# Performance work log

Measured on AMD Instinct MI355X. Metric: run time of the kernel, lower is better.

Reference implementation:

```python
import jax, jax.numpy as jnp
import numpy as np

STOCH, DETER, HID, OBS, ACT = 32, 512, 512, 18, 4
MIN_STD, EPS, UPD_BIAS = 0.1, 1e-3, -1.0


def _ln(x, g, b):
    m = x.mean(-1, keepdims=True)
    v = ((x - m) ** 2).mean(-1, keepdims=True)
    return (x - m) * jax.lax.rsqrt(v + EPS) * g + b


def setup_inputs() -> dict:
    key = jax.random.key(0)
    ks = jax.random.split(key, 10)
    B, T = 256, 256
    def w(k, i, o):
        return jax.random.normal(k, (i, o), jnp.float32) / np.float32(np.sqrt(i))
    return {
        "obs": jax.random.normal(ks[0], (B, T, OBS), jnp.float32),
        "action": jax.random.normal(ks[1], (B, T, ACT), jnp.float32),
        "is_first": jax.random.randint(ks[2], (B, T), 0, 2, jnp.int32),
        "w_prior_in": w(ks[3], STOCH + ACT, HID),
        "g_prior_in": jnp.ones(HID, jnp.float32),
        "bb_prior_in": jnp.zeros(HID, jnp.float32),
        "w_gru": w(ks[4], HID + DETER, 3 * DETER),
        "g_gru": jnp.ones(3 * DETER, jnp.float32),
        "bb_gru": jnp.zeros(3 * DETER, jnp.float32),
        "w_prior_out": w(ks[5], DETER, HID),
        "g_prior_out": jnp.ones(HID, jnp.float32),
        "bb_prior_out": jnp.zeros(HID, jnp.float32),
        "w_prior_stats": w(ks[6], HID, 2 * STOCH),
        "b_prior_stats": jnp.zeros(2 * STOCH, jnp.float32),
        "w_post": w(ks[7], DETER + OBS, HID),
        "g_post": jnp.ones(HID, jnp.float32),
        "bb_post": jnp.zeros(HID, jnp.float32),
        "w_post_stats": w(ks[8], HID, 2 * STOCH),
        "b_post_stats": jnp.zeros(2 * STOCH, jnp.float32),
        "initial_deter": 0.1 * jax.random.normal(ks[9], (1, DETER), jnp.float32),
    }


def reference(obs, action, is_first,
              w_prior_in, g_prior_in, bb_prior_in,
              w_gru, g_gru, bb_gru,
              w_prior_out, g_prior_out, bb_prior_out,
              w_prior_stats, b_prior_stats,
              w_post, g_post, bb_post,
              w_post_stats, b_post_stats,
              initial_deter):
    """RSSM.observe with sample=False. Returns (B, T, 2*(DETER+3*STOCH)):
    concat of post[deter,stoch,mean,std] and prior[deter,stoch,mean,std];
    stoch == mean since dist.mean is used."""
    B = obs.shape[0]
    # learned initial state (identical for every batch row / reset)
    deter0 = jnp.tanh(initial_deter)                                  # (1, DETER)
    h0 = jax.nn.silu(_ln(deter0 @ w_prior_out, g_prior_out, bb_prior_out))
    s0 = h0 @ w_prior_stats + b_prior_stats
    init_mean, _ = jnp.split(s0, 2, axis=-1)                          # (1, STOCH)

    def step(carry, xs):
        deter, stoch = carry
        o_t, a_t, f_t = xs
        mask = (f_t > 0)[:, None]
        deter = jnp.where(mask, deter0, deter)
        stoch = jnp.where(mask, init_mean, stoch)
        a_t = jnp.where(mask, 0.0, a_t)
        # prior_in
        h = jax.nn.silu(_ln(jnp.concatenate([stoch, a_t], -1) @ w_prior_in,
                            g_prior_in, bb_prior_in))
        # GRU cell (depth=1)
        gates = _ln(jnp.concatenate([h, deter], -1) @ w_gru, g_gru, bb_gru)
        r, c, u = jnp.split(gates, 3, axis=-1)
        r = jax.nn.sigmoid(r)
        u = jax.nn.sigmoid(u + UPD_BIAS)
        cand = jax.nn.silu(r * c)
        deter = u * cand + (1.0 - u) * deter
        # prior stats
        h2 = jax.nn.silu(_ln(deter @ w_prior_out, g_prior_out, bb_prior_out))
        ps = h2 @ w_prior_stats + b_prior_stats
        pm, psd = jnp.split(ps, 2, axis=-1)
        psd = jax.nn.softplus(psd) + MIN_STD
        # posterior
        h3 = jax.nn.silu(_ln(jnp.concatenate([deter, o_t], -1) @ w_post,
                             g_post, bb_post))
        qs = h3 @ w_post_stats + b_post_stats
        qm, qsd = jnp.split(qs, 2, axis=-1)
        qsd = jax.nn.softplus(qsd) + MIN_STD
        out = jnp.concatenate([deter, qm, qm, qsd, deter, pm, pm, psd], -1)
        return (deter, qm), out

    carry0 = (jnp.broadcast_to(deter0, (B, DETER)),
              jnp.broadcast_to(init_mean, (B, STOCH)))
    xs = (obs.swapaxes(0, 1), action.swapaxes(0, 1), is_first.swapaxes(0, 1))
    _, ys = jax.lax.scan(step, carry0, xs)   # (T, B, 2*(DETER+3*STOCH))
    return ys.swapaxes(0, 1)
```

## Files before the change

### kernel.cpp

```cpp
#include <hip/hip_runtime.h>
#include <hip/hip_cooperative_groups.h>

namespace cg = cooperative_groups;

#define TT 256
#define GRID 256
#define BDIM 256

typedef unsigned short u16;
typedef unsigned int u32;
typedef __attribute__((ext_vector_type(8))) short bf16x8;
typedef __attribute__((ext_vector_type(4))) float f32x4;

#define GLL(g, l) __builtin_amdgcn_global_load_lds( \
    (const __attribute__((address_space(1))) void*)(g), \
    (__attribute__((address_space(3))) void*)(l), 16, 0, 0)

struct P {
  const float* obs; const float* action; const int* is_first;
  const float* w_prior_in; const float* g_prior_in; const float* bb_prior_in;
  const float* w_gru; const float* g_gru; const float* bb_gru;
  const float* w_prior_out; const float* g_prior_out; const float* bb_prior_out;
  const float* w_prior_stats; const float* b_prior_stats;
  const float* w_post; const float* g_post; const float* bb_post;
  const float* w_post_stats; const float* b_post_stats;
  const float* initial_deter;
  float* out;
  u16 *WgT3;
  u16 *W2T3;
  u16 *WsT3;
  float *deter0, *init_mean;
  int *segb, *segt0, *nact;
  float *deter;
  float *stoch;
  u16 *xg;
  float *gates;
  u16 *dox;
  float *hraw;
  u16 *h2;
  int CH;
};

__device__ __forceinline__ float b2f(u16 u) {
  union { float f; u32 i; } v; v.i = ((u32)u) << 16; return v.f;
}
__device__ __forceinline__ u16 f2b(float f) {
  union { float f; u32 i; } v; v.f = f;
  u32 r = v.i + 0x7FFF + ((v.i >> 16) & 1);
  return (u16)(r >> 16);
}
__device__ __forceinline__ float sigm(float x) { return 1.f / (1.f + __expf(-x)); }
__device__ __forceinline__ float splus(float x) { return x > 15.f ? x : log1pf(__expf(x)); }

__device__ __forceinline__ void h_from_x(const P& p, int i, float xv, int lane) {
  float a0[8];
  #pragma unroll
  for (int c = 0; c < 8; ++c) a0[c] = 0.f;
  #pragma unroll 4
  for (int j = 0; j < 36; ++j) {
    float s = __shfl(xv, j, 64);
    const float* wr = p.w_prior_in + j * 512 + lane;
    #pragma unroll
    for (int c = 0; c < 8; ++c) a0[c] = fmaf(s, wr[c << 6], a0[c]);
  }
  float sm = 0.f, sq = 0.f;
  #pragma unroll
  for (int c = 0; c < 8; ++c) { sm += a0[c]; sq += a0[c] * a0[c]; }
  #pragma unroll
  for (int o = 32; o; o >>= 1) { sm += __shfl_xor(sm, o); sq += __shfl_xor(sq, o); }
  float m = sm * (1.f / 512.f);
  float rs = rsqrtf(sq * (1.f / 512.f) - m * m + 1e-3f);
  size_t rowb = (size_t)i * 3072;
  #pragma unroll
  for (int c = 0; c < 8; ++c) {
    int col = lane + (c << 6);
    float v = (a0[c] - m) * rs * p.g_prior_in[col] + p.bb_prior_in[col];
    v = v * sigm(v);
    u16 hi = f2b(v); u16 lo = f2b(v - b2f(hi));
    p.xg[rowb + col] = hi;
    p.xg[rowb + 1024 + col] = lo;
    p.xg[rowb + 2048 + col] = hi;
  }
}

__global__ void k_weights(P p) {
  const int E1 = 1536 * 1024, E2 = 1024 * 544, E3 = 128 * 1024;
  const int total = E1 + E2 + E3;
  for (int idx = blockIdx.x * blockDim.x + threadIdx.x; idx < total;
       idx += gridDim.x * blockDim.x) {
    float w; u16* dst; int kk, kappa;
    if (idx < E1) {
      int n = idx >> 10; kk = idx & 1023; kappa = 1024;
      w = p.w_gru[kk * 1536 + n];
      dst = p.WgT3 + (size_t)n * 3072;
    } else if (idx < E1 + E2) {
      int t = idx - E1; int n = t / 544; kk = t - n * 544; kappa = 544;
      if (n < 512) w = (kk < 512) ? p.w_prior_out[kk * 512 + n] : 0.f;
      else         w = (kk < 530) ? p.w_post[kk * 512 + (n - 512)] : 0.f;
      dst = p.W2T3 + (size_t)n * 1632;
    } else {
      int t = idx - E1 - E2; int n = t >> 10; kk = t & 1023; kappa = 1024;
      if (n < 64) w = (kk < 512) ? p.w_prior_stats[kk * 64 + n] : 0.f;
      else        w = (kk >= 512) ? p.w_post_stats[(kk - 512) * 64 + (n - 64)] : 0.f;
      dst = p.WsT3 + (size_t)n * 3072;
    }
    u16 hi = f2b(w); u16 lo = f2b(w - b2f(hi));
    dst[kk] = hi; dst[kappa + kk] = hi; dst[2 * kappa + kk] = lo;
  }
}

__global__ void k_init_state(P p) {
  __shared__ float d0s[512], tmp[512], red[256];
  int tid = threadIdx.x;
  for (int n = tid; n < 512; n += 256) { d0s[n] = tanhf(p.initial_deter[n]); p.deter0[n] = d0s[n]; }
  __syncthreads();
  for (int n = tid; n < 512; n += 256) {
    float s = 0.f;
    for (int d = 0; d < 512; ++d) s = fmaf(d0s[d], p.w_prior_out[d * 512 + n], s);
    tmp[n] = s;
  }
  __syncthreads();
  float ls = 0.f, lq = 0.f;
  for (int n = tid; n < 512; n += 256) { ls += tmp[n]; lq += tmp[n] * tmp[n]; }
  red[tid] = ls; __syncthreads();
  for (int s = 128; s; s >>= 1) { if (tid < s) red[tid] += red[tid + s]; __syncthreads(); }
  float m = red[0] * (1.f / 512.f); __syncthreads();
  red[tid] = lq; __syncthreads();
  for (int s = 128; s; s >>= 1) { if (tid < s) red[tid] += red[tid + s]; __syncthreads(); }
  float rs = rsqrtf(red[0] * (1.f / 512.f) - m * m + 1e-3f); __syncthreads();
  for (int n = tid; n < 512; n += 256) {
    float h = (tmp[n] - m) * rs * p.g_prior_out[n] + p.bb_prior_out[n];
    tmp[n] = h * sigm(h);
  }
  __syncthreads();
  if (tid < 32) {
    float s = 0.f;
    for (int d = 0; d < 512; ++d) s = fmaf(tmp[d], p.w_prior_stats[d * 64 + tid], s);
    p.init_mean[tid] = s + p.b_prior_stats[tid];
  }
}

__global__ void k_segments(P p) {
  __shared__ int hist[257], off[258], cur[257];
  int tid = threadIdx.x;
  for (int i = tid; i < 257; i += 256) hist[i] = 0;
  __syncthreads();
  int b = tid;
  { int t = 0;
    while (t < TT) {
      int t0 = t; t++;
      while (t < TT && p.is_first[b * TT + t] == 0) t++;
      atomicAdd(&hist[t - t0], 1);
    } }
  __syncthreads();
  if (tid == 0) {
    int run = 0;
    for (int len = 256; len >= 0; --len) { off[len] = run; run += hist[len]; }
  }
  __syncthreads();
  for (int i = tid; i < 257; i += 256) { cur[i] = off[i]; p.nact[i] = off[i]; }
  __syncthreads();
  { int t = 0;
    while (t < TT) {
      int t0 = t; t++;
      while (t < TT && p.is_first[b * TT + t] == 0) t++;
      int idx = atomicAdd(&cur[t - t0], 1);
      p.segb[idx] = b; p.segt0[idx] = t0;
    } }
}

__device__ void gemm_tiles(const u16* A, int lda, const u16* B, int ldb,
                           float* C, int ldc, int M, int ntn, int K3,
                           u16* lds, int bid, int nb, int tid) {
  const int wave = tid >> 6, lane = tid & 63, quad = lane >> 4, l15 = lane & 15;
  const int wr = (wave & 1) << 6, wc = (wave >> 1) << 6;
  const int ntm = (M + 127) >> 7;
  const int njobs = ntm * ntn;
  const int row0 = tid >> 2, ko0 = (tid & 3) << 3;
  u16* const la0 = lds + (wave << 9);
  u16* const la1 = lds + 2048 + (wave << 9);
  u16* const lb0 = lds + 8192 + (wave << 9);
  u16* const lb1 = lds + 8192 + 2048 + (wave << 9);
  for (int j = bid; j < njobs; j += nb) {
    int tm = j / ntn, tn = j - tm * ntn;
    int r0 = tm << 7, c0 = tn << 7;
    const u16* ga0 = A + (size_t)(r0 + row0) * lda + ko0;
    const u16* ga1 = A + (size_t)(r0 + row0 + 64) * lda + ko0;
    const u16* gb0 = B + (size_t)(c0 + row0) * ldb + ko0;
    const u16* gb1 = B + (size_t)(c0 + row0 + 64) * ldb + ko0;
    f32x4 acc[4][4];
    #pragma unroll
    for (int a = 0; a < 4; ++a)
      #pragma unroll
      for (int bq = 0; bq < 4; ++bq) acc[a][bq] = f32x4{0.f, 0.f, 0.f, 0.f};
    __syncthreads();
    GLL(ga0, la0); GLL(ga1, la1); GLL(gb0, lb0); GLL(gb1, lb1);
    int buf = 0;
    for (int k0 = 0; k0 < K3; k0 += 32) {
      __syncthreads();
      if (k0 + 32 < K3) {
        int bo = (buf ^ 1) << 12;
        int o = k0 + 32;
        GLL(ga0 + o, la0 + bo); GLL(ga1 + o, la1 + bo);
        GLL(gb0 + o, lb0 + bo); GLL(gb1 + o, lb1 + bo);
      }
      const u16* Ab = lds + (buf << 12);
      const u16* Bb = lds + 8192 + (buf << 12);
      bf16x8 af[4], bf[4];
      #pragma unroll
      for (int s2 = 0; s2 < 4; ++s2) {
        af[s2] = *(const bf16x8*)&Ab[((wr + (s2 << 4) + l15) << 5) + (quad << 3)];
        bf[s2] = *(const bf16x8*)&Bb[((wc + (s2 << 4) + l15) << 5) + (quad << 3)];
      }
      #pragma unroll
      for (int mi = 0; mi < 4; ++mi)
        #pragma unroll
        for (int ni = 0; ni < 4; ++ni)
          acc[mi][ni] = __builtin_amdgcn_mfma_f32_16x16x32_bf16(af[mi], bf[ni], acc[mi][ni], 0, 0, 0);
      buf ^= 1;
    }
    #pragma unroll
    for (int mi = 0; mi < 4; ++mi)
      #pragma unroll
      for (int ni = 0; ni < 4; ++ni)
        #pragma unroll
        for (int r = 0; r < 4; ++r)
          C[(size_t)(r0 + wr + (mi << 4) + (quad << 2) + r) * ldc
            + c0 + wc + (ni << 4) + l15] = acc[mi][ni][r];
  }
}

__global__ void __launch_bounds__(BDIM, 2) k_main(P p) {
  cg::grid_group grid = cg::this_grid();
  __shared__ u16 lds[16384];
  const int tid = threadIdx.x;
  const int bid = blockIdx.x, nb = gridDim.x;
  const int wave = tid >> 6, lane = tid & 63, quad = lane >> 4, l15 = lane & 15;
  const int gw = (bid << 2) + wave, nwv = nb << 2;
  const int CH = p.CH;
  const int S_total = p.nact[0];

  for (int base = 0; base < S_total; base += CH) {
    for (int k = 0;; ++k) {
      int Sk = p.nact[k] - base; Sk = Sk > CH ? CH : Sk;
      if (Sk <= 0) break;

      for (int i = gw; i < Sk; i += nwv) {
        int gi = base + i;
        int b = p.segb[gi], t0 = p.segt0[gi];
        float xv = 0.f;
        if (k == 0) {
          size_t rowb = (size_t)i * 3072;
          #pragma unroll
          for (int c = 0; c < 8; ++c) {
            int d = lane + (c << 6);
            float v = p.deter0[d];
            p.deter[(size_t)i * 512 + d] = v;
            u16 hi = f2b(v); u16 lo = f2b(v - b2f(hi));
            p.xg[rowb + 512 + d] = hi;
            p.xg[rowb + 1536 + d] = lo;
            p.xg[rowb + 2560 + d] = hi;
          }
          int ff = p.is_first[b * TT + t0];
          if (lane < 32) xv = p.init_mean[lane];
          else if (lane < 36) xv = (ff > 0) ? 0.f : p.action[((size_t)b * TT + t0) * 4 + (lane - 32)];
        } else {
          if (lane < 32) xv = p.stoch[(size_t)i * 32 + lane];
          else if (lane < 36) xv = p.action[((size_t)b * TT + t0 + k) * 4 + (lane - 32)];
        }
        h_from_x(p, i, xv, lane);
      }
      grid.sync();

      gemm_tiles(p.xg, 3072, p.WgT3, 3072, p.gates, 1536, Sk, 12, 3072,
                 lds, bid, nb, tid);
      grid.sync();

      for (int i = gw; i < Sk; i += nwv) {
        const float* grow = p.gates + (size_t)i * 1536;
        float g[24];
        float sm = 0.f, sq = 0.f;
        #pragma unroll
        for (int c = 0; c < 24; ++c) {
          g[c] = grow[lane + (c << 6)];
          sm += g[c]; sq += g[c] * g[c];
        }
        #pragma unroll
        for (int o = 32; o; o >>= 1) { sm += __shfl_xor(sm, o); sq += __shfl_xor(sq, o); }
        float m = sm * (1.f / 1536.f);
        float rs = rsqrtf(sq * (1.f / 1536.f) - m * m + 1e-3f);
        int gi = base + i;
        int b = p.segb[gi], t = p.segt0[gi] + k;
        float* orow = p.out + ((size_t)b * TT + t) * 1216;
        size_t rowx = (size_t)i * 3072, rowd = (size_t)i * 1632;
        #pragma unroll
        for (int c = 0; c < 8; ++c) {
          int d = lane + (c << 6);
          float gr = (g[c]      - m) * rs * p.g_gru[d]        + p.bb_gru[d];
          float gc = (g[c + 8]  - m) * rs * p.g_gru[512 + d]  + p.bb_gru[512 + d];
          float gu = (g[c + 16] - m) * rs * p.g_gru[1024 + d] + p.bb_gru[1024 + d];
          float r_ = sigm(gr);
          float u_ = sigm(gu - 1.0f);
          float rc = r_ * gc;
          float cand = rc * sigm(rc);
          float dp = p.deter[(size_t)i * 512 + d];
          float dn = u_ * cand + (1.f - u_) * dp;
          p.deter[(size_t)i * 512 + d] = dn;
          orow[d] = dn; orow[608 + d] = dn;
          u16 hi = f2b(dn); u16 lo = f2b(dn - b2f(hi));
          p.xg[rowx + 512 + d] = hi;
          p.xg[rowx + 1536 + d] = lo;
          p.xg[rowx + 2560 + d] = hi;
          p.dox[rowd + d] = hi;
          p.dox[rowd + 544 + d] = lo;
          p.dox[rowd + 1088 + d] = hi;
        }
        if (lane < 32) {
          float ov = (lane < 18) ? p.obs[((size_t)b * TT + t) * 18 + lane] : 0.f;
          u16 hi = f2b(ov); u16 lo = f2b(ov - b2f(hi));
          p.dox[rowd + 512 + lane] = hi;
          p.dox[rowd + 1056 + lane] = lo;
          p.dox[rowd + 1600 + lane] = hi;
        }
      }
      grid.sync();

      gemm_tiles(p.dox, 1632, p.W2T3, 1632, p.hraw, 1024, Sk, 8, 1632,
                 lds, bid, nb, tid);
      grid.sync();

      for (int i = gw; i < Sk; i += nwv) {
        size_t rowh = (size_t)i * 3072;
        #pragma unroll
        for (int hh = 0; hh < 2; ++hh) {
          const float* hb = p.hraw + (size_t)i * 1024 + (hh << 9);
          const float* gv = hh ? p.g_post : p.g_prior_out;
          const float* bv = hh ? p.bb_post : p.bb_prior_out;
          float v[8];
          float sm = 0.f, sq = 0.f;
          #pragma unroll
          for (int c = 0; c < 8; ++c) {
            v[c] = hb[lane + (c << 6)];
            sm += v[c]; sq += v[c] * v[c];
          }
          #pragma unroll
          for (int o = 32; o; o >>= 1) { sm += __shfl_xor(sm, o); sq += __shfl_xor(sq, o); }
          float m = sm * (1.f / 512.f);
          float rs = rsqrtf(sq * (1.f / 512.f) - m * m + 1e-3f);
          #pragma unroll
          for (int c = 0; c < 8; ++c) {
            int d = lane + (c << 6);
            float x = (v[c] - m) * rs * gv[d] + bv[d];
            x = x * sigm(x);
            int col = (hh << 9) + d;
            u16 hi = f2b(x); u16 lo = f2b(x - b2f(hi));
            p.h2[rowh + col] = hi;
            p.h2[rowh + 1024 + col] = lo;
            p.h2[rowh + 2048 + col] = hi;
          }
        }
      }
      grid.sync();

      {
        const int sr = (wave & 1) << 4, sc = (wave >> 1) << 6;
        const int frow = tid >> 2, fko = (tid & 3) << 3;
        int njobs = (Sk + 31) >> 5;
        const u16* gbF0 = p.WsT3 + (size_t)frow * 3072 + fko;
        const u16* gbF1 = p.WsT3 + (size_t)(frow + 64) * 3072 + fko;
        u16* const lFA = lds + (wave << 9);
        u16* const lFB0 = lds + 2048 + (wave << 9);
        u16* const lFB1 = lds + 2048 + 2048 + (wave << 9);
        for (int j = bid; j < njobs; j += nb) {
          int r0 = j << 5;
          const u16* gaF = p.h2 + (size_t)(r0 + frow) * 3072 + fko;
          f32x4 acc[4];
          #pragma unroll
          for (int z = 0; z < 4; ++z) acc[z] = f32x4{0.f, 0.f, 0.f, 0.f};
          __syncthreads();
          if (tid < 128) GLL(gaF, lFA);
          GLL(gbF0, lFB0); GLL(gbF1, lFB1);
          int buf = 0;
          for (int k0 = 0; k0 < 3072; k0 += 32) {
            __syncthreads();
            if (k0 + 32 < 3072) {
              int nbuf = buf ^ 1;
              int o = k0 + 32;
              if (tid < 128) GLL(gaF + o, lFA + (nbuf << 10));
              GLL(gbF0 + o, lFB0 + (nbuf << 12));
              GLL(gbF1 + o, lFB1 + (nbuf << 12));
            }
            const u16* FA = lds + (buf << 10);
            const u16* FB = lds + 2048 + (buf << 12);
            bf16x8 af = *(const bf16x8*)&FA[((sr + l15) << 5) + (quad << 3)];
            #pragma unroll
            for (int ns = 0; ns < 4; ++ns) {
              bf16x8 bf = *(const bf16x8*)&FB[((sc + (ns << 4) + l15) << 5) + (quad << 3)];
              acc[ns] = __builtin_amdgcn_mfma_f32_16x16x32_bf16(af, bf, acc[ns], 0, 0, 0);
            }
            buf ^= 1;
          }
          #pragma unroll
          for (int ns = 0; ns < 4; ++ns)
            #pragma unroll
            for (int r = 0; r < 4; ++r) {
              int i = r0 + sr + (quad << 2) + r;
              int col = sc + (ns << 4) + l15;
              if (i < Sk) {
                float v = acc[ns][r];
                int gi = base + i;
                int b = p.segb[gi], t = p.segt0[gi] + k;
                float* orow = p.out + ((size_t)b * TT + t) * 1216;
                if (col < 32) {
                  v += p.b_prior_stats[col];
                  orow[1120 + col] = v; orow[1152 + col] = v;
                } else if (col < 64) {
                  v = splus(v + p.b_prior_stats[col]) + 0.1f;
                  orow[1184 + col - 32] = v;
                } else if (col < 96) {
                  v += p.b_post_stats[col - 64];
                  orow[512 + col - 64] = v; orow[544 + col - 64] = v;
                  p.stoch[(size_t)i * 32 + (col - 64)] = v;
                } else {
                  v = splus(v + p.b_post_stats[col - 64]) + 0.1f;
                  orow[576 + col - 96] = v;
                }
              }
            }
        }
      }
      grid.sync();
    }
  }
}

extern "C" void kernel_launch(void* const* d_in, const int* in_sizes, int n_in,
                              void* d_out, int out_size, void* d_ws, size_t ws_size,
                              hipStream_t stream) {
  P p;
  p.obs = (const float*)d_in[0];
  p.action = (const float*)d_in[1];
  p.is_first = (const int*)d_in[2];
  p.w_prior_in = (const float*)d_in[3];
  p.g_prior_in = (const float*)d_in[4];
  p.bb_prior_in = (const float*)d_in[5];
  p.w_gru = (const float*)d_in[6];
  p.g_gru = (const float*)d_in[7];
  p.bb_gru = (const float*)d_in[8];
  p.w_prior_out = (const float*)d_in[9];
  p.g_prior_out = (const float*)d_in[10];
  p.bb_prior_out = (const float*)d_in[11];
  p.w_prior_stats = (const float*)d_in[12];
  p.b_prior_stats = (const float*)d_in[13];
  p.w_post = (const float*)d_in[14];
  p.g_post = (const float*)d_in[15];
  p.bb_post = (const float*)d_in[16];
  p.w_post_stats = (const float*)d_in[17];
  p.b_post_stats = (const float*)d_in[18];
  p.initial_deter = (const float*)d_in[19];
  p.out = (float*)d_out;

  char* w = (char*)d_ws;
  auto alloc = [&](size_t bytes) -> char* {
    char* r = w; w += (bytes + 255) & ~(size_t)255; return r;
  };
  p.WgT3 = (u16*)alloc((size_t)1536 * 3072 * 2);
  p.W2T3 = (u16*)alloc((size_t)1024 * 1632 * 2);
  p.WsT3 = (u16*)alloc((size_t)128 * 3072 * 2);
  p.deter0    = (float*)alloc(512 * 4);
  p.init_mean = (float*)alloc(32 * 4);
  p.segb  = (int*)alloc((size_t)65536 * 4);
  p.segt0 = (int*)alloc((size_t)65536 * 4);
  p.nact  = (int*)alloc(257 * 4);
  size_t used = (size_t)(w - (char*)d_ws);
  size_t avail = ws_size > used ? ws_size - used : 0;
  long long ch = (long long)(avail / 28672);
  if (ch > 8192) ch = 8192;
  ch &= ~127LL;
  if (ch < 128) ch = 128;
  p.CH = (int)ch;
  p.deter = (float*)alloc((size_t)p.CH * 512 * 4);
  p.stoch = (float*)alloc((size_t)p.CH * 32 * 4);
  p.xg    = (u16*)alloc((size_t)p.CH * 3072 * 2);
  p.gates = (float*)alloc((size_t)p.CH * 1536 * 4);
  p.dox   = (u16*)alloc((size_t)p.CH * 1632 * 2);
  p.hraw  = (float*)alloc((size_t)p.CH * 1024 * 4);
  p.h2    = (u16*)alloc((size_t)p.CH * 3072 * 2);

  k_weights<<<dim3(256), dim3(256), 0, stream>>>(p);
  k_init_state<<<dim3(1), dim3(256), 0, stream>>>(p);
  k_segments<<<dim3(1), dim3(256), 0, stream>>>(p);
  void* args[] = { &p };
  hipLaunchCooperativeKernel(reinterpret_cast<void*>(&k_main), dim3(GRID), dim3(BDIM),
                             args, 0, stream);
}
```

Before: 10.61 ms.

## Replace grid-synced chunked GEMMs with per-block 32-row tiles from an atomic queue

The cooperative kernel, which ran every timestep with grid-wide syncs and 128x128 GEMM tiles over all active rows, is replaced. Each block now pulls 32-row tiles of sorted segments from an atomic work queue and runs the whole recurrence for them locally, using only block barriers. Weights and activations are pre-laid-out in 32-column K-chunks with an XOR swizzle, and each GEMM uses a triple-buffered global-to-LDS pipeline with explicit vmcnt waits. This removes grid-sync latency but makes every block stream the full weight set for each tile and timestep, which adds weight traffic and leaves load balance to the queue.

```diff
diff --git a/kernel.cpp b/kernel.cpp
--- a/kernel.cpp
+++ b/kernel.cpp
@@ -1,11 +1,8 @@
 #include <hip/hip_runtime.h>
-#include <hip/hip_cooperative_groups.h>
-
-namespace cg = cooperative_groups;
 
 #define TT 256
-#define GRID 256
 #define BDIM 256
+#define MT 32
 
 typedef unsigned short u16;
 typedef unsigned int u32;
@@ -30,15 +27,14 @@
   u16 *W2T3;
   u16 *WsT3;
   float *deter0, *init_mean;
-  int *segb, *segt0, *nact;
+  int *segb, *segt0, *nact, *qhead;
+  u16 *arow;
+  u16 *h2;
+  float *gates;
+  float *hraw;
   float *deter;
   float *stoch;
-  u16 *xg;
-  float *gates;
-  u16 *dox;
-  float *hraw;
-  u16 *h2;
-  int CH;
+  int NB;
 };
 
 __device__ __forceinline__ float b2f(u16 u) {
@@ -52,7 +48,11 @@
 __device__ __forceinline__ float sigm(float x) { return 1.f / (1.f + __expf(-x)); }
 __device__ __forceinline__ float splus(float x) { return x > 15.f ? x : log1pf(__expf(x)); }
 
-__device__ __forceinline__ void h_from_x(const P& p, int i, float xv, int lane) {
+__device__ __forceinline__ void awr(u16* base, int row, int kk, u16 v) {
+  base[((kk >> 5) << 10) + (((row << 5) + (kk & 31)) ^ ((row & 7) << 3))] = v;
+}
+
+__device__ __forceinline__ void h_from_x(const P& p, u16* slotA, int i, float xv, int lane) {
   float a0[8];
   #pragma unroll
   for (int c = 0; c < 8; ++c) a0[c] = 0.f;
@@ -70,42 +70,59 @@
   for (int o = 32; o; o >>= 1) { sm += __shfl_xor(sm, o); sq += __shfl_xor(sq, o); }
   float m = sm * (1.f / 512.f);
   float rs = rsqrtf(sq * (1.f / 512.f) - m * m + 1e-3f);
-  size_t rowb = (size_t)i * 3072;
   #pragma unroll
   for (int c = 0; c < 8; ++c) {
     int col = lane + (c << 6);
     float v = (a0[c] - m) * rs * p.g_prior_in[col] + p.bb_prior_in[col];
     v = v * sigm(v);
     u16 hi = f2b(v); u16 lo = f2b(v - b2f(hi));
-    p.xg[rowb + col] = hi;
-    p.xg[rowb + 1024 + col] = lo;
-    p.xg[rowb + 2048 + col] = hi;
+    awr(slotA, i, 1536 + col, hi);
+    awr(slotA, i, 2048 + col, lo);
+    awr(slotA, i, 2560 + col, hi);
   }
 }
 
 __global__ void k_weights(P p) {
-  const int E1 = 1536 * 1024, E2 = 1024 * 544, E3 = 128 * 1024;
+  const int E1 = 1536 * 3072, E2 = 1024 * 1632, E3 = 128 * 3072;
   const int total = E1 + E2 + E3;
   for (int idx = blockIdx.x * blockDim.x + threadIdx.x; idx < total;
        idx += gridDim.x * blockDim.x) {
-    float w; u16* dst; int kk, kappa;
+    float w; u16* base; size_t dstIdx; int lo_sel;
     if (idx < E1) {
-      int n = idx >> 10; kk = idx & 1023; kappa = 1024;
-      w = p.w_gru[kk * 1536 + n];
-      dst = p.WgT3 + (size_t)n * 3072;
+      int n = idx / 3072, kk = idx - n * 3072;
+      int sub = (kk < 1536) ? kk : kk - 1536;
+      int c = sub & 511, pl = sub >> 9;
+      w = (kk < 1536) ? p.w_gru[(512 + c) * 1536 + n]
+                      : p.w_gru[c * 1536 + n];
+      lo_sel = (pl == 2);
+      base = p.WgT3;
+      dstIdx = (size_t)(kk >> 5) * 49152 + (((n << 5) + (kk & 31)) ^ ((n & 7) << 3));
     } else if (idx < E1 + E2) {
-      int t = idx - E1; int n = t / 544; kk = t - n * 544; kappa = 544;
-      if (n < 512) w = (kk < 512) ? p.w_prior_out[kk * 512 + n] : 0.f;
-      else         w = (kk < 530) ? p.w_post[kk * 512 + (n - 512)] : 0.f;
-      dst = p.W2T3 + (size_t)n * 1632;
+      int t = idx - E1;
+      int n = t / 1632, kk = t - n * 1632;
+      if (kk < 1536) {
+        int c = kk & 511, pl = kk >> 9;
+        w = (n < 512) ? p.w_prior_out[c * 512 + n] : p.w_post[c * 512 + (n - 512)];
+        lo_sel = (pl == 2);
+      } else {
+        int j = kk - 1536; int c = j & 31, pl = j >> 5;
+        w = (n >= 512 && c < 18) ? p.w_post[(512 + c) * 512 + (n - 512)] : 0.f;
+        lo_sel = (pl == 2);
+      }
+      base = p.W2T3;
+      dstIdx = (size_t)(kk >> 5) * 32768 + (((n << 5) + (kk & 31)) ^ ((n & 7) << 3));
     } else {
-      int t = idx - E1 - E2; int n = t >> 10; kk = t & 1023; kappa = 1024;
-      if (n < 64) w = (kk < 512) ? p.w_prior_stats[kk * 64 + n] : 0.f;
-      else        w = (kk >= 512) ? p.w_post_stats[(kk - 512) * 64 + (n - 64)] : 0.f;
-      dst = p.WsT3 + (size_t)n * 3072;
+      int t = idx - E1 - E2;
+      int n = t / 3072, kk = t - n * 3072;
+      int c = kk & 1023, pl = kk >> 10;
+      if (n < 64) w = (c < 512) ? p.w_prior_stats[c * 64 + n] : 0.f;
+      else        w = (c >= 512) ? p.w_post_stats[(c - 512) * 64 + (n - 64)] : 0.f;
+      lo_sel = (pl == 2);
+      base = p.WsT3;
+      dstIdx = (size_t)(kk >> 5) * 4096 + (((n << 5) + (kk & 31)) ^ ((n & 7) << 3));
     }
     u16 hi = f2b(w); u16 lo = f2b(w - b2f(hi));
-    dst[kk] = hi; dst[kappa + kk] = hi; dst[2 * kappa + kk] = lo;
+    base[dstIdx] = lo_sel ? lo : hi;
   }
 }
 
@@ -143,6 +160,7 @@
 __global__ void k_segments(P p) {
   __shared__ int hist[257], off[258], cur[257];
   int tid = threadIdx.x;
+  if (tid == 0) *p.qhead = 0;
   for (int i = tid; i < 257; i += 256) hist[i] = 0;
   __syncthreads();
   int b = tid;
@@ -169,171 +187,206 @@
     } }
 }
 
-__device__ void gemm_tiles(const u16* A, int lda, const u16* B, int ldb,
-                           float* C, int ldc, int M, int ntn, int K3,
-                           u16* lds, int bid, int nb, int tid) {
-  const int wave = tid >> 6, lane = tid & 63, quad = lane >> 4, l15 = lane & 15;
-  const int wr = (wave & 1) << 6, wc = (wave >> 1) << 6;
-  const int ntm = (M + 127) >> 7;
-  const int njobs = ntm * ntn;
-  const int row0 = tid >> 2, ko0 = (tid & 3) << 3;
-  u16* const la0 = lds + (wave << 9);
-  u16* const la1 = lds + 2048 + (wave << 9);
-  u16* const lb0 = lds + 8192 + (wave << 9);
-  u16* const lb1 = lds + 8192 + 2048 + (wave << 9);
-  for (int j = bid; j < njobs; j += nb) {
-    int tm = j / ntn, tn = j - tm * ntn;
-    int r0 = tm << 7, c0 = tn << 7;
-    const u16* ga0 = A + (size_t)(r0 + row0) * lda + ko0;
-    const u16* ga1 = A + (size_t)(r0 + row0 + 64) * lda + ko0;
-    const u16* gb0 = B + (size_t)(c0 + row0) * ldb + ko0;
-    const u16* gb1 = B + (size_t)(c0 + row0 + 64) * ldb + ko0;
-    f32x4 acc[4][4];
+template<int NI, int NSTEPS, int JAT, int JD>
+__device__ __forceinline__ void gemm_pass(
+    const u16* __restrict__ aBase, const u16* __restrict__ wBase,
+    int wStride, int n0, u16* ldsA, u16* ldsW,
+    int wave, int lane, int quad, int l15, f32x4 (&acc)[2][NI]) {
+
+  auto stage = [&](int st, int buf) {
+    int ach = (JAT < NSTEPS && st >= JAT) ? st + JD : st;
+    const u16* aSrc = aBase + ((size_t)ach << 10) + (wave << 9) + (lane << 3);
+    const u16* wSrc = wBase + (size_t)st * wStride + n0 * 32 + (lane << 3);
+    if (wave < 2) GLL(aSrc, ldsA + buf * 1024 + (wave << 9));
     #pragma unroll
-    for (int a = 0; a < 4; ++a)
-      #pragma unroll
-      for (int bq = 0; bq < 4; ++bq) acc[a][bq] = f32x4{0.f, 0.f, 0.f, 0.f};
-    __syncthreads();
-    GLL(ga0, la0); GLL(ga1, la1); GLL(gb0, lb0); GLL(gb1, lb1);
-    int buf = 0;
-    for (int k0 = 0; k0 < K3; k0 += 32) {
-      __syncthreads();
-      if (k0 + 32 < K3) {
-        int bo = (buf ^ 1) << 12;
-        int o = k0 + 32;
-        GLL(ga0 + o, la0 + bo); GLL(ga1 + o, la1 + bo);
-        GLL(gb0 + o, lb0 + bo); GLL(gb1 + o, lb1 + bo);
-      }
-      const u16* Ab = lds + (buf << 12);
-      const u16* Bb = lds + 8192 + (buf << 12);
-      bf16x8 af[4], bf[4];
-      #pragma unroll
-      for (int s2 = 0; s2 < 4; ++s2) {
-        af[s2] = *(const bf16x8*)&Ab[((wr + (s2 << 4) + l15) << 5) + (quad << 3)];
-        bf[s2] = *(const bf16x8*)&Bb[((wc + (s2 << 4) + l15) << 5) + (quad << 3)];
-      }
-      #pragma unroll
-      for (int mi = 0; mi < 4; ++mi)
-        #pragma unroll
-        for (int ni = 0; ni < 4; ++ni)
-          acc[mi][ni] = __builtin_amdgcn_mfma_f32_16x16x32_bf16(af[mi], bf[ni], acc[mi][ni], 0, 0, 0);
-      buf ^= 1;
+    for (int gg = 0; gg < NI; ++gg) {
+      int g = wave * NI + gg;
+      GLL(wSrc + (g << 9), ldsW + buf * 8192 + (g << 9));
+    }
+  };
+  auto compute = [&](int buf) {
+    const u16* A = ldsA + buf * 1024;
+    const u16* W = ldsW + buf * 8192;
+    int xr = (l15 & 7) << 3;
+    bf16x8 af[2];
+    #pragma unroll
+    for (int mi = 0; mi < 2; ++mi) {
+      int r = mi * 16 + l15;
+      af[mi] = *(const bf16x8*)&A[((r << 5) + (quad << 3)) ^ xr];
     }
     #pragma unroll
-    for (int mi = 0; mi < 4; ++mi)
+    for (int ni = 0; ni < NI; ++ni) {
+      int rr = wave * (NI * 16) + ni * 16 + l15;
+      bf16x8 bv = *(const bf16x8*)&W[((rr << 5) + (quad << 3)) ^ xr];
       #pragma unroll
-      for (int ni = 0; ni < 4; ++ni)
-        #pragma unroll
-        for (int r = 0; r < 4; ++r)
-          C[(size_t)(r0 + wr + (mi << 4) + (quad << 2) + r) * ldc
-            + c0 + wc + (ni << 4) + l15] = acc[mi][ni][r];
-  }
-}
-
-__global__ void __launch_bounds__(BDIM, 2) k_main(P p) {
-  cg::grid_group grid = cg::this_grid();
-  __shared__ u16 lds[16384];
+      for (int mi = 0; mi < 2; ++mi)
+        acc[mi][ni] = __builtin_amdgcn_mfma_f32_16x16x32_bf16(af[mi], bv, acc[mi][ni], 0, 0, 0);
+    }
+  };
+
+  stage(0, 0); stage(1, 1);
+  int b3 = 0;
+  for (int st = 0; st < NSTEPS - 1; ++st) {
+    if (wave < 2) asm volatile("s_waitcnt vmcnt(%0)" :: "i"(NI + 1) : "memory");
+    else          asm volatile("s_waitcnt vmcnt(%0)" :: "i"(NI) : "memory");
+    __builtin_amdgcn_s_barrier();
+    __builtin_amdgcn_sched_barrier(0);
+    if (st + 2 < NSTEPS) {
+      int bs = b3 + 2; if (bs >= 3) bs -= 3;
+      stage(st + 2, bs);
+    }
+    compute(b3);
+    ++b3; if (b3 == 3) b3 = 0;
+  }
+  asm volatile("s_waitcnt vmcnt(0)" ::: "memory");
+  __builtin_amdgcn_s_barrier();
+  __builtin_amdgcn_sched_barrier(0);
+  compute(b3);
+}
+
+__global__ void __launch_bounds__(BDIM) k_main(P p) {
+  __shared__ u16 lds[27648];
+  __shared__ int sg;
   const int tid = threadIdx.x;
-  const int bid = blockIdx.x, nb = gridDim.x;
   const int wave = tid >> 6, lane = tid & 63, quad = lane >> 4, l15 = lane & 15;
-  const int gw = (bid << 2) + wave, nwv = nb << 2;
-  const int CH = p.CH;
+  u16* ldsA = lds;
+  u16* ldsW = lds + 3072;
+  const int blk = blockIdx.x;
+  u16* slotA = p.arow + (size_t)blk * 102400;
+  u16* slotH = p.h2 + (size_t)blk * 98304;
+  float* slotG = p.gates + (size_t)blk * 49152;
+  float* slotR = p.hraw + (size_t)blk * 32768;
+  float* slotD = p.deter + (size_t)blk * 16384;
+  float* slotS = p.stoch + (size_t)blk * 1024;
   const int S_total = p.nact[0];
-
-  for (int base = 0; base < S_total; base += CH) {
+  const int ntiles = (S_total + MT - 1) >> 5;
+
+  for (;;) {
+    __syncthreads();
+    if (tid == 0) sg = atomicAdd(p.qhead, 1);
+    __syncthreads();
+    int g = sg;
+    if (g >= ntiles) return;
+    int row0 = g * MT;
+    int nr0 = S_total - row0; if (nr0 > MT) nr0 = MT;
+
     for (int k = 0;; ++k) {
-      int Sk = p.nact[k] - base; Sk = Sk > CH ? CH : Sk;
-      if (Sk <= 0) break;
-
-      for (int i = gw; i < Sk; i += nwv) {
-        int gi = base + i;
+      int Mk = p.nact[k] - row0; if (Mk > nr0) Mk = nr0;
+      if (Mk <= 0) break;
+
+      for (int i = wave; i < Mk; i += 4) {
+        int gi = row0 + i;
         int b = p.segb[gi], t0 = p.segt0[gi];
         float xv = 0.f;
         if (k == 0) {
-          size_t rowb = (size_t)i * 3072;
           #pragma unroll
           for (int c = 0; c < 8; ++c) {
             int d = lane + (c << 6);
             float v = p.deter0[d];
-            p.deter[(size_t)i * 512 + d] = v;
+            slotD[i * 512 + d] = v;
             u16 hi = f2b(v); u16 lo = f2b(v - b2f(hi));
-            p.xg[rowb + 512 + d] = hi;
-            p.xg[rowb + 1536 + d] = lo;
-            p.xg[rowb + 2560 + d] = hi;
+            awr(slotA, i, d, hi);
+            awr(slotA, i, 512 + d, lo);
+            awr(slotA, i, 1024 + d, hi);
           }
           int ff = p.is_first[b * TT + t0];
           if (lane < 32) xv = p.init_mean[lane];
           else if (lane < 36) xv = (ff > 0) ? 0.f : p.action[((size_t)b * TT + t0) * 4 + (lane - 32)];
         } else {
-          if (lane < 32) xv = p.stoch[(size_t)i * 32 + lane];
+          if (lane < 32) xv = slotS[i * 32 + lane];
           else if (lane < 36) xv = p.action[((size_t)b * TT + t0 + k) * 4 + (lane - 32)];
         }
-        h_from_x(p, i, xv, lane);
-      }
-      grid.sync();
-
-      gemm_tiles(p.xg, 3072, p.WgT3, 3072, p.gates, 1536, Sk, 12, 3072,
-                 lds, bid, nb, tid);
-      grid.sync();
-
-      for (int i = gw; i < Sk; i += nwv) {
-        const float* grow = p.gates + (size_t)i * 1536;
-        float g[24];
+        h_from_x(p, slotA, i, xv, lane);
+      }
+      __syncthreads();
+
+      for (int np = 0; np < 6; ++np) {
+        f32x4 acc[2][4];
+        #pragma unroll
+        for (int a = 0; a < 2; ++a)
+          #pragma unroll
+          for (int bq = 0; bq < 4; ++bq) acc[a][bq] = f32x4{0.f, 0.f, 0.f, 0.f};
+        gemm_pass<4, 96, 1000, 0>(slotA, p.WgT3, 49152, np * 256,
+                                  ldsA, ldsW, wave, lane, quad, l15, acc);
+        #pragma unroll
+        for (int mi = 0; mi < 2; ++mi)
+          #pragma unroll
+          for (int ni = 0; ni < 4; ++ni)
+            #pragma unroll
+            for (int r = 0; r < 4; ++r)
+              slotG[(mi * 16 + quad * 4 + r) * 1536 + np * 256 + wave * 64 + ni * 16 + l15]
+                  = acc[mi][ni][r];
+      }
+      __syncthreads();
+
+      for (int i = wave; i < Mk; i += 4) {
+        const float* grow = slotG + i * 1536;
+        float g24[24];
         float sm = 0.f, sq = 0.f;
         #pragma unroll
         for (int c = 0; c < 24; ++c) {
-          g[c] = grow[lane + (c << 6)];
-          sm += g[c]; sq += g[c] * g[c];
+          g24[c] = grow[lane + (c << 6)];
+          sm += g24[c]; sq += g24[c] * g24[c];
         }
         #pragma unroll
         for (int o = 32; o; o >>= 1) { sm += __shfl_xor(sm, o); sq += __shfl_xor(sq, o); }
         float m = sm * (1.f / 1536.f);
         float rs = rsqrtf(sq * (1.f / 1536.f) - m * m + 1e-3f);
-        int gi = base + i;
+        int gi = row0 + i;
         int b = p.segb[gi], t = p.segt0[gi] + k;
         float* orow = p.out + ((size_t)b * TT + t) * 1216;
-        size_t rowx = (size_t)i * 3072, rowd = (size_t)i * 1632;
         #pragma unroll
         for (int c = 0; c < 8; ++c) {
           int d = lane + (c << 6);
-          float gr = (g[c]      - m) * rs * p.g_gru[d]        + p.bb_gru[d];
-          float gc = (g[c + 8]  - m) * rs * p.g_gru[512 + d]  + p.bb_gru[512 + d];
-          float gu = (g[c + 16] - m) * rs * p.g_gru[1024 + d] + p.bb_gru[1024 + d];
+          float gr = (g24[c] - m) * rs * p.g_gru[d] + p.bb_gru[d];
+          float gc = (g24[c + 8] - m) * rs * p.g_gru[512 + d] + p.bb_gru[512 + d];
+          float gu = (g24[c + 16] - m) * rs * p.g_gru[1024 + d] + p.bb_gru[1024 + d];
           float r_ = sigm(gr);
           float u_ = sigm(gu - 1.0f);
           float rc = r_ * gc;
           float cand = rc * sigm(rc);
-          float dp = p.deter[(size_t)i * 512 + d];
+          float dp = slotD[i * 512 + d];
           float dn = u_ * cand + (1.f - u_) * dp;
-          p.deter[(size_t)i * 512 + d] = dn;
+          slotD[i * 512 + d] = dn;
           orow[d] = dn; orow[608 + d] = dn;
           u16 hi = f2b(dn); u16 lo = f2b(dn - b2f(hi));
-          p.xg[rowx + 512 + d] = hi;
-          p.xg[rowx + 1536 + d] = lo;
-          p.xg[rowx + 2560 + d] = hi;
-          p.dox[rowd + d] = hi;
-          p.dox[rowd + 544 + d] = lo;
-          p.dox[rowd + 1088 + d] = hi;
+          awr(slotA, i, d, hi);
+          awr(slotA, i, 512 + d, lo);
+          awr(slotA, i, 1024 + d, hi);
         }
         if (lane < 32) {
           float ov = (lane < 18) ? p.obs[((size_t)b * TT + t) * 18 + lane] : 0.f;
           u16 hi = f2b(ov); u16 lo = f2b(ov - b2f(hi));
-          p.dox[rowd + 512 + lane] = hi;
-          p.dox[rowd + 1056 + lane] = lo;
-          p.dox[rowd + 1600 + lane] = hi;
+          awr(slotA, i, 3072 + lane, hi);
+          awr(slotA, i, 3104 + lane, lo);
+          awr(slotA, i, 3136 + lane, hi);
         }
       }
-      grid.sync();
-
-      gemm_tiles(p.dox, 1632, p.W2T3, 1632, p.hraw, 1024, Sk, 8, 1632,
-                 lds, bid, nb, tid);
-      grid.sync();
-
-      for (int i = gw; i < Sk; i += nwv) {
-        size_t rowh = (size_t)i * 3072;
+      __syncthreads();
+
+      for (int np = 0; np < 4; ++np) {
+        f32x4 acc[2][4];
+        #pragma unroll
+        for (int a = 0; a < 2; ++a)
+          #pragma unroll
+          for (int bq = 0; bq < 4; ++bq) acc[a][bq] = f32x4{0.f, 0.f, 0.f, 0.f};
+        gemm_pass<4, 51, 48, 48>(slotA, p.W2T3, 32768, np * 256,
+                                 ldsA, ldsW, wave, lane, quad, l15, acc);
+        #pragma unroll
+        for (int mi = 0; mi < 2; ++mi)
+          #pragma unroll
+          for (int ni = 0; ni < 4; ++ni)
+            #pragma unroll
+            for (int r = 0; r < 4; ++r)
+              slotR[(mi * 16 + quad * 4 + r) * 1024 + np * 256 + wave * 64 + ni * 16 + l15]
+                  = acc[mi][ni][r];
+      }
+      __syncthreads();
+
+      for (int i = wave; i < Mk; i += 4) {
         #pragma unroll
         for (int hh = 0; hh < 2; ++hh) {
-          const float* hb = p.hraw + (size_t)i * 1024 + (hh << 9);
+          const float* hb = slotR + i * 1024 + (hh << 9);
           const float* gv = hh ? p.g_post : p.g_prior_out;
           const float* bv = hh ? p.bb_post : p.bb_prior_out;
           float v[8];
@@ -354,61 +407,33 @@
             x = x * sigm(x);
             int col = (hh << 9) + d;
             u16 hi = f2b(x); u16 lo = f2b(x - b2f(hi));
-            p.h2[rowh + col] = hi;
-            p.h2[rowh + 1024 + col] = lo;
-            p.h2[rowh + 2048 + col] = hi;
+            awr(slotH, i, col, hi);
+            awr(slotH, i, 1024 + col, lo);
+            awr(slotH, i, 2048 + col, hi);
           }
         }
       }
-      grid.sync();
+      __syncthreads();
 
       {
-        const int sr = (wave & 1) << 4, sc = (wave >> 1) << 6;
-        const int frow = tid >> 2, fko = (tid & 3) << 3;
-        int njobs = (Sk + 31) >> 5;
-        const u16* gbF0 = p.WsT3 + (size_t)frow * 3072 + fko;
-        const u16* gbF1 = p.WsT3 + (size_t)(frow + 64) * 3072 + fko;
-        u16* const lFA = lds + (wave << 9);
-        u16* const lFB0 = lds + 2048 + (wave << 9);
-        u16* const lFB1 = lds + 2048 + 2048 + (wave << 9);
-        for (int j = bid; j < njobs; j += nb) {
-          int r0 = j << 5;
-          const u16* gaF = p.h2 + (size_t)(r0 + frow) * 3072 + fko;
-          f32x4 acc[4];
-          #pragma unroll
-          for (int z = 0; z < 4; ++z) acc[z] = f32x4{0.f, 0.f, 0.f, 0.f};
-          __syncthreads();
-          if (tid < 128) GLL(gaF, lFA);
-          GLL(gbF0, lFB0); GLL(gbF1, lFB1);
-          int buf = 0;
-          for (int k0 = 0; k0 < 3072; k0 += 32) {
-            __syncthreads();
-            if (k0 + 32 < 3072) {
-              int nbuf = buf ^ 1;
-              int o = k0 + 32;
-              if (tid < 128) GLL(gaF + o, lFA + (nbuf << 10));
-              GLL(gbF0 + o, lFB0 + (nbuf << 12));
-              GLL(gbF1 + o, lFB1 + (nbuf << 12));
-            }
-            const u16* FA = lds + (buf << 10);
-            const u16* FB = lds + 2048 + (buf << 12);
-            bf16x8 af = *(const bf16x8*)&FA[((sr + l15) << 5) + (quad << 3)];
-            #pragma unroll
-            for (int ns = 0; ns < 4; ++ns) {
-              bf16x8 bf = *(const bf16x8*)&FB[((sc + (ns << 4) + l15) << 5) + (quad << 3)];
-              acc[ns] = __builtin_amdgcn_mfma_f32_16x16x32_bf16(af, bf, acc[ns], 0, 0, 0);
-            }
-            buf ^= 1;
-          }
-          #pragma unroll
-          for (int ns = 0; ns < 4; ++ns)
+        f32x4 acc[2][2];
+        #pragma unroll
+        for (int a = 0; a < 2; ++a)
+          #pragma unroll
+          for (int bq = 0; bq < 2; ++bq) acc[a][bq] = f32x4{0.f, 0.f, 0.f, 0.f};
+        gemm_pass<2, 96, 1000, 0>(slotH, p.WsT3, 4096, 0,
+                                  ldsA, ldsW, wave, lane, quad, l15, acc);
+        #pragma unroll
+        for (int mi = 0; mi < 2; ++mi)
+          #pragma unroll
+          for (int ni = 0; ni < 2; ++ni)
             #pragma unroll
             for (int r = 0; r < 4; ++r) {
-              int i = r0 + sr + (quad << 2) + r;
-              int col = sc + (ns << 4) + l15;
-              if (i < Sk) {
-                float v = acc[ns][r];
-                int gi = base + i;
+              int i = mi * 16 + quad * 4 + r;
+              int col = wave * 32 + ni * 16 + l15;
+              if (i < Mk) {
+                float v = acc[mi][ni][r];
+                int gi = row0 + i;
                 int b = p.segb[gi], t = p.segt0[gi] + k;
                 float* orow = p.out + ((size_t)b * TT + t) * 1216;
                 if (col < 32) {
@@ -420,16 +445,15 @@
                 } else if (col < 96) {
                   v += p.b_post_stats[col - 64];
                   orow[512 + col - 64] = v; orow[544 + col - 64] = v;
-                  p.stoch[(size_t)i * 32 + (col - 64)] = v;
+                  slotS[i * 32 + (col - 64)] = v;
                 } else {
                   v = splus(v + p.b_post_stats[col - 64]) + 0.1f;
                   orow[576 + col - 96] = v;
                 }
               }
             }
-        }
-      }
-      grid.sync();
+      }
+      __syncthreads();
     }
   }
 }
@@ -467,30 +491,28 @@
   p.WgT3 = (u16*)alloc((size_t)1536 * 3072 * 2);
   p.W2T3 = (u16*)alloc((size_t)1024 * 1632 * 2);
   p.WsT3 = (u16*)alloc((size_t)128 * 3072 * 2);
-  p.deter0    = (float*)alloc(512 * 4);
+  p.deter0 = (float*)alloc(512 * 4);
   p.init_mean = (float*)alloc(32 * 4);
-  p.segb  = (int*)alloc((size_t)65536 * 4);
+  p.segb = (int*)alloc((size_t)65536 * 4);
   p.segt0 = (int*)alloc((size_t)65536 * 4);
-  p.nact  = (int*)alloc(257 * 4);
+  p.nact = (int*)alloc(257 * 4);
+  p.qhead = (int*)alloc(256);
   size_t used = (size_t)(w - (char*)d_ws);
   size_t avail = ws_size > used ? ws_size - used : 0;
-  long long ch = (long long)(avail / 28672);
-  if (ch > 8192) ch = 8192;
-  ch &= ~127LL;
-  if (ch < 128) ch = 128;
-  p.CH = (int)ch;
-  p.deter = (float*)alloc((size_t)p.CH * 512 * 4);
-  p.stoch = (float*)alloc((size_t)p.CH * 32 * 4);
-  p.xg    = (u16*)alloc((size_t)p.CH * 3072 * 2);
-  p.gates = (float*)alloc((size_t)p.CH * 1536 * 4);
-  p.dox   = (u16*)alloc((size_t)p.CH * 1632 * 2);
-  p.hraw  = (float*)alloc((size_t)p.CH * 1024 * 4);
-  p.h2    = (u16*)alloc((size_t)p.CH * 3072 * 2);
+  size_t slot = 800768;
+  long long nb = (long long)(avail / slot);
+  if (nb > 256) nb = 256;
+  if (nb < 1) nb = 1;
+  p.NB = (int)nb;
+  p.arow = (u16*)alloc((size_t)p.NB * 204800);
+  p.h2 = (u16*)alloc((size_t)p.NB * 196608);
+  p.gates = (float*)alloc((size_t)p.NB * 196608);
+  p.hraw = (float*)alloc((size_t)p.NB * 131072);
+  p.deter = (float*)alloc((size_t)p.NB * 65536);
+  p.stoch = (float*)alloc((size_t)p.NB * 4096);
 
   k_weights<<<dim3(256), dim3(256), 0, stream>>>(p);
   k_init_state<<<dim3(1), dim3(256), 0, stream>>>(p);
   k_segments<<<dim3(1), dim3(256), 0, stream>>>(p);
-  void* args[] = { &p };
-  hipLaunchCooperativeKernel(reinterpret_cast<void*>(&k_main), dim3(GRID), dim3(BDIM),
-                             args, 0, stream);
-}
+  k_main<<<dim3(p.NB), dim3(BDIM), 0, stream>>>(p);
+}
```

Result: slower. 13.90 ms (+31.1%).
